# Performance work log

Hardware: AMD Instinct MI355X
Metric: run time of the kernel (lower is better)

The kernel has to match this reference:

```python
import jax, jax.numpy as jnp
import numpy as np

HEAD_DIM = 128
NEG = -1e9


def setup_inputs() -> dict:
    key = jax.random.key(0)
    kq, kk, kv, kl = jax.random.split(key, 4)
    B, S, D = 8, 2048, HEAD_DIM
    q = jax.random.normal(kq, (B, S, D), dtype=jnp.float32)
    k = jax.random.normal(kk, (B, S, D), dtype=jnp.float32)
    v = jax.random.normal(kv, (B, S, D), dtype=jnp.float32)
    event_length = jax.random.randint(kl, (B,), 0, 2048, dtype=jnp.int32)
    return {"q": q, "k": k, "v": v, "event_length": event_length}


def reference(q, k, v, event_length):
    B, S, D = q.shape
    scale = jnp.sqrt(jnp.asarray(D, dtype=q.dtype))
    # [B, S, S] attention scores
    scores = jnp.einsum("bsd,btd->bst", q, k) / scale
    idx = jnp.arange(S)
    valid = idx[None, :] < event_length[:, None]          # [B, S]
    mask = valid[:, :, None] & valid[:, None, :]          # [B, S, S]
    scores = jnp.where(mask, scores, jnp.asarray(NEG, dtype=scores.dtype))
    attn = jax.nn.softmax(scores, axis=-1)
    # dropout is eval-mode identity
    return jnp.einsum("bst,btd->bsd", attn, v)
```

## Files before the change

kernel.cpp:

```cpp
#include <hip/hip_runtime.h>

#define S 2048
#define D 128
#define BATCH 8
#define KSTR 136
#define VSTR 72

typedef _Float16 half8 __attribute__((ext_vector_type(8)));
typedef _Float16 half4_t __attribute__((ext_vector_type(4)));
typedef float f4 __attribute__((ext_vector_type(4)));

__device__ __forceinline__ half8 cvt8(f4 a, f4 b) {
    half8 h;
    h[0] = (_Float16)a[0]; h[1] = (_Float16)a[1];
    h[2] = (_Float16)a[2]; h[3] = (_Float16)a[3];
    h[4] = (_Float16)b[0]; h[5] = (_Float16)b[1];
    h[6] = (_Float16)b[2]; h[7] = (_Float16)b[3];
    return h;
}

__global__ __launch_bounds__(256) void k_prep(const float* __restrict__ kin,
                                              const float* __restrict__ v,
                                              _Float16* __restrict__ kh,
                                              _Float16* __restrict__ vt,
                                              float* __restrict__ part) {
    int bid = blockIdx.x;
    int b = bid & 7, c = bid >> 3, tid = threadIdx.x;
    size_t off = ((size_t)b * S + c * 32) * D;
    #pragma unroll
    for (int p = 0; p < 2; ++p) {
        size_t i = (size_t)p * 2048 + tid * 8;
        f4 a = *(const f4*)(kin + off + i);
        f4 bb = *(const f4*)(kin + off + i + 4);
        *(half8*)(kh + off + i) = cvt8(a, bb);
    }
    __shared__ float tile[32 * 132];
    __shared__ f4 sred[256][2];
    f4 a0 = {0.f, 0.f, 0.f, 0.f}, a1 = {0.f, 0.f, 0.f, 0.f};
    int d0 = (tid & 15) * 8;
    #pragma unroll
    for (int p = 0; p < 2; ++p) {
        int t = p * 16 + (tid >> 4);
        f4 x = *(const f4*)(v + off + (size_t)t * D + d0);
        f4 y = *(const f4*)(v + off + (size_t)t * D + d0 + 4);
        a0 += x; a1 += y;
        *(f4*)&tile[t * 132 + d0] = x;
        *(f4*)&tile[t * 132 + d0 + 4] = y;
    }
    sred[tid][0] = a0; sred[tid][1] = a1;
    __syncthreads();
    if (tid < 16) {
        f4 s0 = sred[tid][0], s1 = sred[tid][1];
        for (int g = 1; g < 16; ++g) { s0 += sred[g * 16 + tid][0]; s1 += sred[g * 16 + tid][1]; }
        float* dst = part + ((size_t)b * 64 + c) * 128 + tid * 8;
        *(f4*)dst = s0;
        *(f4*)(dst + 4) = s1;
    }
    int u = tid & 3, dd = tid >> 2;
    #pragma unroll
    for (int pass = 0; pass < 2; ++pass) {
        int d = pass * 64 + dd;
        half8 h;
        #pragma unroll
        for (int i = 0; i < 8; ++i) h[i] = (_Float16)tile[(u * 8 + i) * 132 + d];
        *(half8*)(vt + ((size_t)(b * D + d)) * S + c * 32 + u * 8) = h;
    }
}

__global__ __launch_bounds__(256, 4) void k_attn(
    const float* __restrict__ q, const _Float16* __restrict__ kh,
    const _Float16* __restrict__ vt, const int* __restrict__ el,
    const float* __restrict__ part, float* __restrict__ out) {
    int bid = blockIdx.x;
    int rg = bid >> 3;
    int b = (bid + rg) & 7;
    int Lb = el[b], m0 = rg * 32;
    int tid = threadIdx.x;
    const float inv_s = 1.0f / (float)S;

    __shared__ __align__(16) char smem[35840];
    _Float16* Kh = (_Float16*)smem;
    _Float16* Vt = (_Float16*)(smem + 17408);
    float* cmb  = (float*)smem;
    float* psb  = (float*)(smem + 16896);
    float* vsum = (float*)(smem + 17024);

    if (m0 >= Lb) {
        if (tid < 128) {
            float s = 0.f;
            const float* pp = part + (size_t)b * 64 * 128 + tid;
            #pragma unroll 4
            for (int c = 0; c < 64; ++c) s += pp[c * 128];
            vsum[tid] = s * inv_s;
        }
        __syncthreads();
        int r = tid >> 3, d0 = (tid & 7) * 16;
        float* orow = out + ((size_t)b * S + m0 + r) * D + d0;
        #pragma unroll
        for (int i = 0; i < 4; ++i) *(f4*)(orow + i * 4) = *(const f4*)(vsum + d0 + i * 4);
        return;
    }
    int nkt = (Lb + 63) >> 6;

    int lane = tid & 63, w = tid >> 6;
    int h = w >> 1, wl = w & 1;
    int col = lane & 15, quad = lane >> 4;

    const float scale = 0.0883883476483184f;
    half8 qf[4];
    {
        const float* qb = q + ((size_t)b * S + m0 + wl * 16 + col) * D;
        #pragma unroll
        for (int kc = 0; kc < 4; ++kc) {
            f4 a = *(const f4*)(qb + kc * 32 + quad * 8);
            f4 b2 = *(const f4*)(qb + kc * 32 + quad * 8 + 4);
            a *= scale; b2 *= scale;
            qf[kc] = cvt8(a, b2);
        }
    }

    f4 O[8];
    #pragma unroll
    for (int i = 0; i < 8; ++i) O[i] = (f4){0.f, 0.f, 0.f, 0.f};
    float ps = 0.f;

    int kr = tid >> 4, kc8 = (tid & 15) << 3;
    int vr = tid >> 3, vc8 = (tid & 7) << 3;
    const _Float16* kb_ = kh + (size_t)b * S * D;
    const _Float16* vb_ = vt + (size_t)b * D * S;

    half8 kreg[4], vreg[4];
    {
        #pragma unroll
        for (int p = 0; p < 4; ++p)
            kreg[p] = *(const half8*)(kb_ + (size_t)(p * 16 + kr) * D + kc8);
        #pragma unroll
        for (int p = 0; p < 4; ++p)
            vreg[p] = *(const half8*)(vb_ + (size_t)(p * 32 + vr) * S + vc8);
        #pragma unroll
        for (int p = 0; p < 4; ++p)
            *(half8*)&Kh[(p * 16 + kr) * KSTR + kc8] = kreg[p];
        #pragma unroll
        for (int p = 0; p < 4; ++p)
            *(half8*)&Vt[(p * 32 + vr) * VSTR + vc8] = vreg[p];
    }
    __syncthreads();

    for (int kt = 0; kt < nkt; ++kt) {
        int t0 = kt * 64;
        bool hasnext = (kt + 1) < nkt;
        if (hasnext) {
            int tn = t0 + 64;
            #pragma unroll
            for (int p = 0; p < 4; ++p)
                kreg[p] = *(const half8*)(kb_ + (size_t)(tn + p * 16 + kr) * D + kc8);
            #pragma unroll
            for (int p = 0; p < 4; ++p)
                vreg[p] = *(const half8*)(vb_ + (size_t)(p * 32 + vr) * S + tn + vc8);
        }

        #pragma unroll
        for (int nt2 = 0; nt2 < 2; ++nt2) {
            int nt = h * 2 + nt2;
            f4 sa = {0.f, 0.f, 0.f, 0.f};
            __builtin_amdgcn_s_setprio(1);
            #pragma unroll
            for (int kc = 0; kc < 4; ++kc) {
                half8 kf = *(const half8*)&Kh[(nt * 16 + col) * KSTR + kc * 32 + quad * 8];
                sa = __builtin_amdgcn_mfma_f32_16x16x32_f16(kf, qf[kc], sa, 0, 0, 0);
            }
            __builtin_amdgcn_s_setprio(0);
            int tq = t0 + nt * 16 + quad * 4;
            half4_t ph;
            #pragma unroll
            for (int r = 0; r < 4; ++r) {
                float e = (tq + r < Lb) ? __expf(fminf(sa[r], 10.0f)) : 0.f;
                ps += e;
                ph[r] = (_Float16)e;
            }
            __builtin_amdgcn_s_setprio(1);
            #pragma unroll
            for (int dt = 0; dt < 8; ++dt) {
                half4_t vf = *(const half4_t*)&Vt[(dt * 16 + col) * VSTR + nt * 16 + quad * 4];
                O[dt] = __builtin_amdgcn_mfma_f32_16x16x16f16(ph, vf, O[dt], 0, 0, 0);
            }
            __builtin_amdgcn_s_setprio(0);
        }

        if (hasnext) {
            __syncthreads();
            #pragma unroll
            for (int p = 0; p < 4; ++p)
                *(half8*)&Kh[(p * 16 + kr) * KSTR + kc8] = kreg[p];
            #pragma unroll
            for (int p = 0; p < 4; ++p)
                *(half8*)&Vt[(p * 32 + vr) * VSTR + vc8] = vreg[p];
            __syncthreads();
        }
    }

    __syncthreads();
    bool tail = (m0 + 32 > Lb);
    if (tail && tid < 128) {
        float s = 0.f;
        const float* pp = part + (size_t)b * 64 * 128 + tid;
        #pragma unroll 4
        for (int c = 0; c < 64; ++c) s += pp[c * 128];
        vsum[tid] = s * inv_s;
    }
    ps += __shfl_xor(ps, 16, 64);
    ps += __shfl_xor(ps, 32, 64);

    if (h == 0) {
        #pragma unroll
        for (int dt = 0; dt < 8; ++dt)
            #pragma unroll
            for (int r = 0; r < 4; ++r)
                cmb[(wl * 16 + quad * 4 + r) * 132 + dt * 16 + col] = O[dt][r];
        if (quad == 0) psb[wl * 16 + col] = ps;
    }
    __syncthreads();
    if (h == 1) {
        #pragma unroll
        for (int dt = 0; dt < 8; ++dt)
            #pragma unroll
            for (int r = 0; r < 4; ++r)
                atomicAdd(&cmb[(wl * 16 + quad * 4 + r) * 132 + dt * 16 + col], O[dt][r]);
        if (quad == 0) atomicAdd(&psb[wl * 16 + col], ps);
    }
    __syncthreads();
    if (h == 0) {
        float pst = psb[wl * 16 + col];
        float l4[4];
        #pragma unroll
        for (int r = 0; r < 4; ++r) l4[r] = __shfl(pst, quad * 4 + r, 64);

        float smv[8] = {};
        if (tail) {
            #pragma unroll
            for (int dt = 0; dt < 8; ++dt) smv[dt] = vsum[dt * 16 + col];
        }
        #pragma unroll
        for (int r = 0; r < 4; ++r) {
            int row = m0 + wl * 16 + quad * 4 + r;
            float inv = 1.0f / l4[r];
            float* orow = out + ((size_t)b * S + row) * D;
            #pragma unroll
            for (int dt = 0; dt < 8; ++dt) {
                float val = (row < Lb)
                    ? cmb[(wl * 16 + quad * 4 + r) * 132 + dt * 16 + col] * inv
                    : smv[dt];
                orow[dt * 16 + col] = val;
            }
        }
    }
}

extern "C" void kernel_launch(void* const* d_in, const int* in_sizes, int n_in,
                              void* d_out, int out_size, void* d_ws, size_t ws_size,
                              hipStream_t stream) {
    const float* q = (const float*)d_in[0];
    const float* k = (const float*)d_in[1];
    const float* v = (const float*)d_in[2];
    const int* el = (const int*)d_in[3];
    float* out = (float*)d_out;

    const size_t SZ_PART = (size_t)BATCH * 64 * 128 * 4;
    const size_t SZ_HALF = (size_t)BATCH * D * S * 2;
    float* part = (float*)d_ws;
    _Float16* kh = (_Float16*)((char*)d_ws + SZ_PART);
    _Float16* vt = (_Float16*)((char*)d_ws + SZ_PART + SZ_HALF);

    k_prep<<<dim3(512), 256, 0, stream>>>(k, v, kh, vt, part);
    k_attn<<<dim3(512), 256, 0, stream>>>(q, kh, vt, el, part, out);
}
```

Measured before the change: 125.7 us.

## Enlarge attention blocks to 64 rows with four-way intra-block KV split

The attention kernel now launches 256 blocks of 1024 threads. Each block covers 64 query rows, and four 256-thread groups process interleaved 64-key tiles, each group with its own shared-memory K/V buffers. The partial outputs and softmax sums are then combined through shared-memory atomics. The aim is to halve global K/V traffic per query row and raise per-block parallelism. In exchange, each block uses about 140 KB of LDS (one block per CU), barriers span 16 waves, and coarser blocks may worsen load balance across batches of very different lengths.

```diff
diff --git a/kernel.cpp b/kernel.cpp
--- a/kernel.cpp
+++ b/kernel.cpp
@@ -5,6 +5,7 @@
 #define BATCH 8
 #define KSTR 136
 #define VSTR 72
+#define QSZ 35840
 
 typedef _Float16 half8 __attribute__((ext_vector_type(8)));
 typedef _Float16 half4_t __attribute__((ext_vector_type(4)));
@@ -67,49 +68,51 @@
     }
 }
 
-__global__ __launch_bounds__(256, 4) void k_attn(
+__global__ __launch_bounds__(1024, 4) void k_attn(
     const float* __restrict__ q, const _Float16* __restrict__ kh,
     const _Float16* __restrict__ vt, const int* __restrict__ el,
     const float* __restrict__ part, float* __restrict__ out) {
     int bid = blockIdx.x;
-    int rg = bid >> 3;
-    int b = (bid + rg) & 7;
-    int Lb = el[b], m0 = rg * 32;
+    int b = bid & 7, mg = bid >> 3;
+    int Lb = el[b], m0 = mg * 64;
     int tid = threadIdx.x;
     const float inv_s = 1.0f / (float)S;
 
-    __shared__ __align__(16) char smem[35840];
-    _Float16* Kh = (_Float16*)smem;
-    _Float16* Vt = (_Float16*)(smem + 17408);
-    float* cmb  = (float*)smem;
-    float* psb  = (float*)(smem + 16896);
-    float* vsum = (float*)(smem + 17024);
+    __shared__ __align__(16) char smem[4 * QSZ];
 
     if (m0 >= Lb) {
+        float* vsum0 = (float*)smem;
         if (tid < 128) {
             float s = 0.f;
             const float* pp = part + (size_t)b * 64 * 128 + tid;
             #pragma unroll 4
             for (int c = 0; c < 64; ++c) s += pp[c * 128];
-            vsum[tid] = s * inv_s;
+            vsum0[tid] = s * inv_s;
         }
         __syncthreads();
-        int r = tid >> 3, d0 = (tid & 7) * 16;
+        int r = tid >> 4, d0 = (tid & 15) * 8;
         float* orow = out + ((size_t)b * S + m0 + r) * D + d0;
-        #pragma unroll
-        for (int i = 0; i < 4; ++i) *(f4*)(orow + i * 4) = *(const f4*)(vsum + d0 + i * 4);
+        *(f4*)orow = *(const f4*)(vsum0 + d0);
+        *(f4*)(orow + 4) = *(const f4*)(vsum0 + d0 + 4);
         return;
     }
     int nkt = (Lb + 63) >> 6;
-
-    int lane = tid & 63, w = tid >> 6;
-    int h = w >> 1, wl = w & 1;
+    int NT = (nkt + 3) >> 2;
+
+    int q4 = tid >> 8, tid4 = tid & 255;
+    int lane = tid & 63, w4 = tid4 >> 6;
     int col = lane & 15, quad = lane >> 4;
+
+    _Float16* Kh = (_Float16*)(smem + q4 * QSZ);
+    _Float16* Vt = (_Float16*)(smem + q4 * QSZ + 17408);
+    float* cmb  = (float*)smem;
+    float* psb  = (float*)(smem + 33792);
+    float* vsum = (float*)(smem + 34048);
 
     const float scale = 0.0883883476483184f;
     half8 qf[4];
     {
-        const float* qb = q + ((size_t)b * S + m0 + wl * 16 + col) * D;
+        const float* qb = q + ((size_t)b * S + m0 + w4 * 16 + col) * D;
         #pragma unroll
         for (int kc = 0; kc < 4; ++kc) {
             f4 a = *(const f4*)(qb + kc * 32 + quad * 8);
@@ -124,19 +127,20 @@
     for (int i = 0; i < 8; ++i) O[i] = (f4){0.f, 0.f, 0.f, 0.f};
     float ps = 0.f;
 
-    int kr = tid >> 4, kc8 = (tid & 15) << 3;
-    int vr = tid >> 3, vc8 = (tid & 7) << 3;
+    int kr = tid4 >> 4, kc8 = (tid4 & 15) << 3;
+    int vr = tid4 >> 3, vc8 = (tid4 & 7) << 3;
     const _Float16* kb_ = kh + (size_t)b * S * D;
     const _Float16* vb_ = vt + (size_t)b * D * S;
 
     half8 kreg[4], vreg[4];
-    {
-        #pragma unroll
-        for (int p = 0; p < 4; ++p)
-            kreg[p] = *(const half8*)(kb_ + (size_t)(p * 16 + kr) * D + kc8);
-        #pragma unroll
-        for (int p = 0; p < 4; ++p)
-            vreg[p] = *(const half8*)(vb_ + (size_t)(p * 32 + vr) * S + vc8);
+    if (q4 < nkt) {
+        int t0 = q4 * 64;
+        #pragma unroll
+        for (int p = 0; p < 4; ++p)
+            kreg[p] = *(const half8*)(kb_ + (size_t)(t0 + p * 16 + kr) * D + kc8);
+        #pragma unroll
+        for (int p = 0; p < 4; ++p)
+            vreg[p] = *(const half8*)(vb_ + (size_t)(p * 32 + vr) * S + t0 + vc8);
         #pragma unroll
         for (int p = 0; p < 4; ++p)
             *(half8*)&Kh[(p * 16 + kr) * KSTR + kc8] = kreg[p];
@@ -146,11 +150,15 @@
     }
     __syncthreads();
 
-    for (int kt = 0; kt < nkt; ++kt) {
-        int t0 = kt * 64;
-        bool hasnext = (kt + 1) < nkt;
-        if (hasnext) {
-            int tn = t0 + 64;
+    for (int s = 0; s < NT; ++s) {
+        int kt = s * 4 + q4;
+        bool valid = kt < nkt;
+        bool morestep = (s + 1) < NT;
+        int ktn = kt + 4;
+        bool vnext = ktn < nkt;
+
+        if (morestep && vnext) {
+            int tn = ktn * 64;
             #pragma unroll
             for (int p = 0; p < 4; ++p)
                 kreg[p] = *(const half8*)(kb_ + (size_t)(tn + p * 16 + kr) * D + kc8);
@@ -159,48 +167,55 @@
                 vreg[p] = *(const half8*)(vb_ + (size_t)(p * 32 + vr) * S + tn + vc8);
         }
 
-        #pragma unroll
-        for (int nt2 = 0; nt2 < 2; ++nt2) {
-            int nt = h * 2 + nt2;
-            f4 sa = {0.f, 0.f, 0.f, 0.f};
-            __builtin_amdgcn_s_setprio(1);
-            #pragma unroll
-            for (int kc = 0; kc < 4; ++kc) {
-                half8 kf = *(const half8*)&Kh[(nt * 16 + col) * KSTR + kc * 32 + quad * 8];
-                sa = __builtin_amdgcn_mfma_f32_16x16x32_f16(kf, qf[kc], sa, 0, 0, 0);
+        if (valid) {
+            int t0 = kt * 64;
+            #pragma unroll
+            for (int nt = 0; nt < 4; ++nt) {
+                f4 sa = {0.f, 0.f, 0.f, 0.f};
+                __builtin_amdgcn_s_setprio(1);
+                #pragma unroll
+                for (int kc = 0; kc < 4; ++kc) {
+                    half8 kf = *(const half8*)&Kh[(nt * 16 + col) * KSTR + kc * 32 + quad * 8];
+                    sa = __builtin_amdgcn_mfma_f32_16x16x32_f16(kf, qf[kc], sa, 0, 0, 0);
+                }
+                __builtin_amdgcn_s_setprio(0);
+                int tq = t0 + nt * 16 + quad * 4;
+                half4_t ph;
+                #pragma unroll
+                for (int r = 0; r < 4; ++r) {
+                    float e = (tq + r < Lb) ? __expf(fminf(sa[r], 10.0f)) : 0.f;
+                    ps += e;
+                    ph[r] = (_Float16)e;
+                }
+                __builtin_amdgcn_s_setprio(1);
+                #pragma unroll
+                for (int dt = 0; dt < 8; ++dt) {
+                    half4_t vf = *(const half4_t*)&Vt[(dt * 16 + col) * VSTR + nt * 16 + quad * 4];
+                    O[dt] = __builtin_amdgcn_mfma_f32_16x16x16f16(ph, vf, O[dt], 0, 0, 0);
+                }
+                __builtin_amdgcn_s_setprio(0);
             }
-            __builtin_amdgcn_s_setprio(0);
-            int tq = t0 + nt * 16 + quad * 4;
-            half4_t ph;
-            #pragma unroll
-            for (int r = 0; r < 4; ++r) {
-                float e = (tq + r < Lb) ? __expf(fminf(sa[r], 10.0f)) : 0.f;
-                ps += e;
-                ph[r] = (_Float16)e;
+        }
+
+        if (morestep) {
+            __syncthreads();
+            if (vnext) {
+                #pragma unroll
+                for (int p = 0; p < 4; ++p)
+                    *(half8*)&Kh[(p * 16 + kr) * KSTR + kc8] = kreg[p];
+                #pragma unroll
+                for (int p = 0; p < 4; ++p)
+                    *(half8*)&Vt[(p * 32 + vr) * VSTR + vc8] = vreg[p];
             }
-            __builtin_amdgcn_s_setprio(1);
-            #pragma unroll
-            for (int dt = 0; dt < 8; ++dt) {
-                half4_t vf = *(const half4_t*)&Vt[(dt * 16 + col) * VSTR + nt * 16 + quad * 4];
-                O[dt] = __builtin_amdgcn_mfma_f32_16x16x16f16(ph, vf, O[dt], 0, 0, 0);
-            }
-            __builtin_amdgcn_s_setprio(0);
-        }
-
-        if (hasnext) {
             __syncthreads();
-            #pragma unroll
-            for (int p = 0; p < 4; ++p)
-                *(half8*)&Kh[(p * 16 + kr) * KSTR + kc8] = kreg[p];
-            #pragma unroll
-            for (int p = 0; p < 4; ++p)
-                *(half8*)&Vt[(p * 32 + vr) * VSTR + vc8] = vreg[p];
-            __syncthreads();
-        }
-    }
-
-    __syncthreads();
-    bool tail = (m0 + 32 > Lb);
+        }
+    }
+
+    __syncthreads();
+    ps += __shfl_xor(ps, 16, 64);
+    ps += __shfl_xor(ps, 32, 64);
+
+    bool tail = (m0 + 64 > Lb);
     if (tail && tid < 128) {
         float s = 0.f;
         const float* pp = part + (size_t)b * 64 * 128 + tid;
@@ -208,29 +223,26 @@
         for (int c = 0; c < 64; ++c) s += pp[c * 128];
         vsum[tid] = s * inv_s;
     }
-    ps += __shfl_xor(ps, 16, 64);
-    ps += __shfl_xor(ps, 32, 64);
-
-    if (h == 0) {
+    if (q4 == 0) {
         #pragma unroll
         for (int dt = 0; dt < 8; ++dt)
             #pragma unroll
             for (int r = 0; r < 4; ++r)
-                cmb[(wl * 16 + quad * 4 + r) * 132 + dt * 16 + col] = O[dt][r];
-        if (quad == 0) psb[wl * 16 + col] = ps;
-    }
-    __syncthreads();
-    if (h == 1) {
+                cmb[(w4 * 16 + quad * 4 + r) * 132 + dt * 16 + col] = O[dt][r];
+        if (quad == 0) psb[w4 * 16 + col] = ps;
+    }
+    __syncthreads();
+    if (q4 != 0) {
         #pragma unroll
         for (int dt = 0; dt < 8; ++dt)
             #pragma unroll
             for (int r = 0; r < 4; ++r)
-                atomicAdd(&cmb[(wl * 16 + quad * 4 + r) * 132 + dt * 16 + col], O[dt][r]);
-        if (quad == 0) atomicAdd(&psb[wl * 16 + col], ps);
-    }
-    __syncthreads();
-    if (h == 0) {
-        float pst = psb[wl * 16 + col];
+                atomicAdd(&cmb[(w4 * 16 + quad * 4 + r) * 132 + dt * 16 + col], O[dt][r]);
+        if (quad == 0) atomicAdd(&psb[w4 * 16 + col], ps);
+    }
+    __syncthreads();
+    if (q4 == 0) {
+        float pst = psb[w4 * 16 + col];
         float l4[4];
         #pragma unroll
         for (int r = 0; r < 4; ++r) l4[r] = __shfl(pst, quad * 4 + r, 64);
@@ -242,13 +254,13 @@
         }
         #pragma unroll
         for (int r = 0; r < 4; ++r) {
-            int row = m0 + wl * 16 + quad * 4 + r;
+            int row = m0 + w4 * 16 + quad * 4 + r;
             float inv = 1.0f / l4[r];
             float* orow = out + ((size_t)b * S + row) * D;
             #pragma unroll
             for (int dt = 0; dt < 8; ++dt) {
                 float val = (row < Lb)
-                    ? cmb[(wl * 16 + quad * 4 + r) * 132 + dt * 16 + col] * inv
+                    ? cmb[(w4 * 16 + quad * 4 + r) * 132 + dt * 16 + col] * inv
                     : smv[dt];
                 orow[dt * 16 + col] = val;
             }
@@ -272,5 +284,5 @@
     _Float16* vt = (_Float16*)((char*)d_ws + SZ_PART + SZ_HALF);
 
     k_prep<<<dim3(512), 256, 0, stream>>>(k, v, kh, vt, part);
-    k_attn<<<dim3(512), 256, 0, stream>>>(q, kh, vt, el, part, out);
-}
+    k_attn<<<dim3(256), 1024, 0, stream>>>(q, kh, vt, el, part, out);
+}
```

Result: slower. 141.5 us (+12.5%).
